# Performance work log

Measured on AMD Instinct MI355X. Metric: run time of the kernel, lower is better.

## Reference

```python
import math
import jax, jax.numpy as jnp
import numpy as np

D = 1024
B, L = 4, 4096


def _linear(x, W, b):
    # torch nn.Linear convention: y = x @ W.T + b, W: (out, in)
    return jnp.einsum('bld,ed->ble', x, W) + b


def _ma_k_activation(x, k=0.02):
    x = x / math.sqrt(x.shape[-1])
    return jax.nn.sigmoid(x * k)


def _ma_q_activation(x):
    x = -x / math.sqrt(x.shape[-1])
    return -jnp.where(x >= 0, x, 0.02 * x)  # -leaky_relu(x, 0.02)


def setup_inputs() -> dict:
    key = jax.random.key(0)
    ks = jax.random.split(key, 9)
    s = 1.0 / math.sqrt(D)
    return {
        'x': jax.random.normal(ks[0], (B, L, D), dtype=jnp.float32),
        'Wq1': jax.random.uniform(ks[1], (D, D), jnp.float32, -s, s),
        'bq1': jax.random.uniform(ks[2], (D,), jnp.float32, -s, s),
        'Wk1': jax.random.uniform(ks[3], (D, D), jnp.float32, -s, s),
        'bk1': jax.random.uniform(ks[4], (D,), jnp.float32, -s, s),
        'Wk2': jax.random.uniform(ks[5], (D, D), jnp.float32, -s, s),
        'bk2': jax.random.uniform(ks[6], (D,), jnp.float32, -s, s),
        'Wproj': jax.random.uniform(ks[7], (D, D), jnp.float32, -s, s),
        'bproj': jax.random.uniform(ks[8], (D,), jnp.float32, -s, s),
    }


def reference(x, Wq1, bq1, Wk1, bk1, Wk2, bk2, Wproj, bproj):
    V = x
    # AR branch: exponential keys, normalized running average, sigmoid query gate
    K = jnp.exp(_linear(x, Wk1, bk1))                      # (B,L,D)
    K_cum = jnp.cumsum(K, axis=1) + 1e-6
    S = jnp.cumsum(K * V, axis=1) / K_cum
    Q = jax.nn.sigmoid(_linear(x, Wq1, bq1))
    O_ar = S * Q
    # MA branch: residual errors gated by shifted (q,k) activations
    zero = jnp.zeros_like(x[:, :1, :])
    E = jnp.concatenate([zero, V[:, 1:, :] - O_ar[:, :-1, :]], axis=1)
    qk2_in = jnp.concatenate([zero, x[:, :-1, :]], axis=1)
    K2 = _ma_k_activation(_linear(qk2_in, Wk2, bk2))
    S2 = jnp.cumsum(K2 * E, axis=1)
    Q2 = _ma_q_activation(Q)
    Q2 = jnp.concatenate([zero, Q2[:, :-1, :]], axis=1)
    O_ma = S2 * Q2
    return _linear(O_ar + O_ma, Wproj, bproj)
```

## Files before the change

### kernel.cpp

```cpp
#include <hip/hip_runtime.h>

#define D_DIM 1024
#define L_DIM 4096
#define B_DIM 4
#define M_DIM (B_DIM * L_DIM)
#define N1    3072
#define KDIM  1024
#define NKT   16
#define KAPPA 6.25e-4f

using f32x4  = __attribute__((ext_vector_type(4))) float;
using bf16x8 = __attribute__((ext_vector_type(8))) short;

__device__ __forceinline__ unsigned short f2bf(float f) {
    unsigned u = __float_as_uint(f);
    u += 0x7fffu + ((u >> 16) & 1u);
    return (unsigned short)(u >> 16);
}
__device__ __forceinline__ float bf2f(unsigned short h) {
    return __uint_as_float(((unsigned)h) << 16);
}
__device__ __forceinline__ float bflo(unsigned u) { return __uint_as_float(u << 16); }
__device__ __forceinline__ float bfhi(unsigned u) { return __uint_as_float(u & 0xffff0000u); }
__device__ __forceinline__ unsigned pack2(float a, float b) {
    return (unsigned)f2bf(a) | ((unsigned)f2bf(b) << 16);
}
__device__ __forceinline__ float sigmoidf_(float x) {
    return 1.0f / (1.0f + __expf(-x));
}

__global__ void cvt_bf16_kernel(const float* __restrict__ in, unsigned short* __restrict__ out, int n) {
    int i = (blockIdx.x * blockDim.x + threadIdx.x) * 4;
    if (i < n) {
        float4 v = *reinterpret_cast<const float4*>(in + i);
        uint2 p;
        p.x = pack2(v.x, v.y);
        p.y = pack2(v.z, v.w);
        *reinterpret_cast<uint2*>(out + i) = p;
    }
}

__global__ void cvt4_bf16_kernel(const float* __restrict__ w0, const float* __restrict__ w1,
                                 const float* __restrict__ w2, const float* __restrict__ w3,
                                 unsigned short* __restrict__ out) {
    int seg = blockIdx.x >> 10;
    int lb  = blockIdx.x & 1023;
    int i   = (lb * 256 + threadIdx.x) * 4;
    const float* src = (seg == 0) ? w0 : (seg == 1) ? w1 : (seg == 2) ? w2 : w3;
    float4 v = *reinterpret_cast<const float4*>(src + i);
    uint2 p;
    p.x = pack2(v.x, v.y);
    p.y = pack2(v.z, v.w);
    *reinterpret_cast<uint2*>(out + seg * 1048576 + i) = p;
}

__device__ __forceinline__ void gld_lds16(const void* g, void* s) {
    __builtin_amdgcn_global_load_lds((const __attribute__((address_space(1))) void*)g,
                                     (__attribute__((address_space(3))) void*)s, 16, 0, 0);
}

#define BAR()  do { asm volatile("" ::: "memory"); __builtin_amdgcn_s_barrier(); asm volatile("" ::: "memory"); } while (0)
#define MFMA16(a_, b_, c_) __builtin_amdgcn_mfma_f32_16x16x32_bf16(a_, b_, c_, 0, 0, 0)

__global__ __launch_bounds__(512, 2) void gemm256(
        const unsigned short* __restrict__ A, const unsigned short* __restrict__ Bm,
        unsigned short* __restrict__ Cb, float* __restrict__ Cf,
        const float* __restrict__ bb0, const float* __restrict__ bb1, const float* __restrict__ bb2,
        int nwgDiv8, int mode) {
    extern __shared__ __align__(16) short lds[];
    const int tid  = threadIdx.x;
    const int wid  = tid >> 6, lane = tid & 63;
    const int wr   = wid >> 2, wc = wid & 3;
    const int lr   = lane & 15, kg = lane >> 4;

    int lin = blockIdx.y * 64 + blockIdx.x;
    int swz = (lin & 7) * nwgDiv8 + (lin >> 3);
    int bm = swz & 63;
    int bn = swz >> 6;
    const size_t rowA0 = (size_t)bm * 256;
    const size_t rowB0 = (size_t)bn * 256;

    const int rh = tid >> 2;
    const int sl = (tid & 3) ^ ((rh >> 1) & 3);
    const int wbase = (tid >> 6) * 512;
    const size_t aoffG = (size_t)rh * KDIM + sl * 8;

#define STAGE(Mp_, row0_, kt_, kh_, c_, mat_, cur_) \
    gld_lds16((Mp_) + ((row0_) + (size_t)(c_) * 128) * KDIM + (size_t)(kt_) * 64 + (kh_) * 32 + aoffG, \
              (void*)(lds + (cur_) * 32768 + (mat_) * 16384 + (kh_) * 8192 + (c_) * 4096 + wbase))

    const int slotR = kg ^ ((lr >> 1) & 3);
    const int aRd = (wr * 128 + lr) * 32 + slotR * 8;
    const int bRd = (wc * 64  + lr) * 32 + slotR * 8;

    f32x4 acc[8][4];
#pragma unroll
    for (int i = 0; i < 8; ++i)
#pragma unroll
        for (int j = 0; j < 4; ++j) acc[i][j] = (f32x4){0.f, 0.f, 0.f, 0.f};

    STAGE(A,  rowA0, 0, 0, 0, 0, 0); STAGE(A,  rowA0, 0, 0, 1, 0, 0);
    STAGE(Bm, rowB0, 0, 0, 0, 1, 0); STAGE(Bm, rowB0, 0, 0, 1, 1, 0);
    STAGE(A,  rowA0, 0, 1, 0, 0, 0); STAGE(A,  rowA0, 0, 1, 1, 0, 0);
    STAGE(Bm, rowB0, 0, 1, 0, 1, 0); STAGE(Bm, rowB0, 0, 1, 1, 1, 0);
    STAGE(A,  rowA0, 1, 0, 0, 0, 1); STAGE(A,  rowA0, 1, 0, 1, 0, 1);
    STAGE(Bm, rowB0, 1, 0, 0, 1, 1); STAGE(Bm, rowB0, 1, 0, 1, 1, 1);
    asm volatile("s_waitcnt vmcnt(4)" ::: "memory");
    BAR();

    for (int kt = 0; kt < NKT; ++kt) {
        const int cur = kt & 1;
        const int nc  = cur ^ 1;
        const short* A0 = lds + cur * 32768;
        const short* A1 = A0 + 8192;
        const short* B0 = A0 + 16384;
        const short* B1 = A0 + 24576;
        bf16x8 a[8], b0, b1, b2, b3;

        #pragma unroll
        for (int fm = 0; fm < 8; ++fm) a[fm] = *reinterpret_cast<const bf16x8*>(A0 + aRd + fm * 512);
        b0 = *reinterpret_cast<const bf16x8*>(B0 + bRd);
        b1 = *reinterpret_cast<const bf16x8*>(B0 + bRd + 512);
        if (kt + 1 < NKT) {
            STAGE(A, rowA0, kt + 1, 1, 0, 0, nc); STAGE(A, rowA0, kt + 1, 1, 1, 0, nc);
        }
        BAR();
        __builtin_amdgcn_s_setprio(1);
        #pragma unroll
        for (int fm = 0; fm < 8; ++fm) {
            acc[fm][0] = MFMA16(b0, a[fm], acc[fm][0]);
            acc[fm][1] = MFMA16(b1, a[fm], acc[fm][1]);
        }
        __builtin_amdgcn_s_setprio(0);
        BAR();

        b2 = *reinterpret_cast<const bf16x8*>(B0 + bRd + 1024);
        b3 = *reinterpret_cast<const bf16x8*>(B0 + bRd + 1536);
        if (kt + 1 < NKT) {
            STAGE(Bm, rowB0, kt + 1, 1, 0, 1, nc); STAGE(Bm, rowB0, kt + 1, 1, 1, 1, nc);
        }
        BAR();
        __builtin_amdgcn_s_setprio(1);
        #pragma unroll
        for (int fm = 0; fm < 8; ++fm) {
            acc[fm][2] = MFMA16(b2, a[fm], acc[fm][2]);
            acc[fm][3] = MFMA16(b3, a[fm], acc[fm][3]);
        }
        __builtin_amdgcn_s_setprio(0);
        BAR();

        #pragma unroll
        for (int fm = 0; fm < 8; ++fm) a[fm] = *reinterpret_cast<const bf16x8*>(A1 + aRd + fm * 512);
        b0 = *reinterpret_cast<const bf16x8*>(B1 + bRd);
        b1 = *reinterpret_cast<const bf16x8*>(B1 + bRd + 512);
        if (kt + 2 < NKT) {
            STAGE(A, rowA0, kt + 2, 0, 0, 0, cur); STAGE(A, rowA0, kt + 2, 0, 1, 0, cur);
        }
        BAR();
        __builtin_amdgcn_s_setprio(1);
        #pragma unroll
        for (int fm = 0; fm < 8; ++fm) {
            acc[fm][0] = MFMA16(b0, a[fm], acc[fm][0]);
            acc[fm][1] = MFMA16(b1, a[fm], acc[fm][1]);
        }
        __builtin_amdgcn_s_setprio(0);
        BAR();

        b2 = *reinterpret_cast<const bf16x8*>(B1 + bRd + 1024);
        b3 = *reinterpret_cast<const bf16x8*>(B1 + bRd + 1536);
        if (kt + 2 < NKT) {
            STAGE(Bm, rowB0, kt + 2, 0, 0, 1, cur); STAGE(Bm, rowB0, kt + 2, 0, 1, 1, cur);
        }
        BAR();
        __builtin_amdgcn_s_setprio(1);
        #pragma unroll
        for (int fm = 0; fm < 8; ++fm) {
            acc[fm][2] = MFMA16(b2, a[fm], acc[fm][2]);
            acc[fm][3] = MFMA16(b3, a[fm], acc[fm][3]);
        }
        __builtin_amdgcn_s_setprio(0);
        if (kt < NKT - 2) { asm volatile("s_waitcnt vmcnt(4)" ::: "memory"); }
        else              { asm volatile("s_waitcnt vmcnt(0)" ::: "memory"); }
        BAR();
    }

    const int rowBase = bm * 256 + wr * 128;
    const int colBase = bn * 256 + wc * 64;
    if (mode == 0) {
        const int seg = (colBase >> 10);
        const float* bs = (seg == 0) ? bb0 : ((seg == 1) ? bb1 : bb2);
#pragma unroll
        for (int fm = 0; fm < 8; ++fm) {
            int row = rowBase + fm * 16 + lr;
            unsigned short* cp = Cb + (size_t)row * 3072;
#pragma unroll
            for (int fn = 0; fn < 4; ++fn) {
                int col0 = colBase + fn * 16 + kg * 4;
                float4 b4 = *reinterpret_cast<const float4*>(bs + (col0 & 1023));
                float v0 = acc[fm][fn][0] + b4.x;
                float v1 = acc[fm][fn][1] + b4.y;
                float v2 = acc[fm][fn][2] + b4.z;
                float v3 = acc[fm][fn][3] + b4.w;
                float r0, r1, r2, r3;
                if (seg == 0)      { r0 = __expf(v0); r1 = __expf(v1); r2 = __expf(v2); r3 = __expf(v3); }
                else if (seg == 1) { r0 = sigmoidf_(v0); r1 = sigmoidf_(v1); r2 = sigmoidf_(v2); r3 = sigmoidf_(v3); }
                else               { r0 = sigmoidf_(v0 * KAPPA); r1 = sigmoidf_(v1 * KAPPA);
                                     r2 = sigmoidf_(v2 * KAPPA); r3 = sigmoidf_(v3 * KAPPA); }
                uint2 p;
                p.x = pack2(r0, r1);
                p.y = pack2(r2, r3);
                *reinterpret_cast<uint2*>(cp + col0) = p;
            }
        }
    } else {
#pragma unroll
        for (int fm = 0; fm < 8; ++fm) {
            int row = rowBase + fm * 16 + lr;
            float* cp = Cf + (size_t)row * 1024;
#pragma unroll
            for (int fn = 0; fn < 4; ++fn) {
                int col0 = colBase + fn * 16 + kg * 4;
                float4 b4 = *reinterpret_cast<const float4*>(bb0 + col0);
                float4 v;
                v.x = acc[fm][fn][0] + b4.x;
                v.y = acc[fm][fn][1] + b4.y;
                v.z = acc[fm][fn][2] + b4.z;
                v.w = acc[fm][fn][3] + b4.w;
                *reinterpret_cast<float4*>(cp + col0) = v;
            }
        }
    }
#undef STAGE
}


__global__ __launch_bounds__(256) void pass1v(
        const unsigned short* __restrict__ KQ, const unsigned short* __restrict__ xbf,
        float2* __restrict__ pK, float2* __restrict__ pKV) {
    const int thr = threadIdx.x;
    const int dq = blockIdx.x & 1;
    const int bc = blockIdx.x >> 1;
    const int b = bc >> 6, c = bc & 63;
    const int d0 = dq * 512 + thr * 2;
    const size_t row0 = (size_t)b * L_DIM + (size_t)c * 64;
    const unsigned short* kp = KQ  + row0 * 3072 + d0;
    const unsigned short* vp = xbf + row0 * 1024 + d0;
    float sK0 = 0.f, sK1 = 0.f, sKV0 = 0.f, sKV1 = 0.f;
#pragma unroll 8
    for (int t = 0; t < 64; ++t) {
        unsigned ku = *reinterpret_cast<const unsigned*>(kp + (size_t)t * 3072);
        unsigned vu = *reinterpret_cast<const unsigned*>(vp + (size_t)t * 1024);
        sK0 += bflo(ku); sK1 += bfhi(ku);
        sKV0 += bflo(ku) * bflo(vu); sKV1 += bfhi(ku) * bfhi(vu);
    }
    const size_t slot = (size_t)bc * 512 + dq * 256 + thr;
    pK[slot]  = make_float2(sK0, sK1);
    pKV[slot] = make_float2(sKV0, sKV1);
}

__global__ __launch_bounds__(256) void pass3v(
        const unsigned short* __restrict__ KQ, const unsigned short* __restrict__ xbf,
        const float2* __restrict__ pK, const float2* __restrict__ pKV,
        unsigned short* __restrict__ z, float2* __restrict__ pM) {
    const int thr = threadIdx.x;
    const int dq = blockIdx.x & 1;
    const int bc = blockIdx.x >> 1;
    const int b = bc >> 6, c = bc & 63;
    const int d0 = dq * 512 + thr * 2;
    const size_t row0 = (size_t)b * L_DIM + (size_t)c * 64;
    const unsigned short* kqp = KQ  + row0 * 3072 + d0;
    const unsigned short* vp  = xbf + row0 * 1024 + d0;
    unsigned short* zp = z + row0 * 1024 + d0;

    float cK0 = 0.f, cK1 = 0.f, cKV0 = 0.f, cKV1 = 0.f;
    const size_t base = (size_t)(b << 6) * 512 + dq * 256 + thr;
#pragma unroll 4
    for (int cp = 0; cp < c; ++cp) {
        float2 a = pK [base + (size_t)cp * 512];
        float2 q2 = pKV[base + (size_t)cp * 512];
        cK0 += a.x; cK1 += a.y; cKV0 += q2.x; cKV1 += q2.y;
    }

    float oar_prev0 = 0.f, oar_prev1 = 0.f, k2_prev0 = 0.f, k2_prev1 = 0.f;
    float q_prev0 = 0.f, q_prev1 = 0.f;
    if (c != 0) {
        unsigned qm  = *reinterpret_cast<const unsigned*>(kqp - 3072 + 1024);
        unsigned k2m = *reinterpret_cast<const unsigned*>(kqp - 3072 + 2048);
        oar_prev0 = bflo(qm) * (cKV0 / (cK0 + 1e-6f));
        oar_prev1 = bfhi(qm) * (cKV1 / (cK1 + 1e-6f));
        k2_prev0 = bflo(k2m); k2_prev1 = bfhi(k2m);
        q_prev0 = bflo(qm);   q_prev1 = bfhi(qm);
    }
    float sM0 = 0.f, sM1 = 0.f;
#pragma unroll 4
    for (int t = 0; t < 64; ++t) {
        unsigned ku  = *reinterpret_cast<const unsigned*>(kqp + (size_t)t * 3072);
        unsigned qu  = *reinterpret_cast<const unsigned*>(kqp + (size_t)t * 3072 + 1024);
        unsigned k2u = *reinterpret_cast<const unsigned*>(kqp + (size_t)t * 3072 + 2048);
        unsigned vu  = *reinterpret_cast<const unsigned*>(vp  + (size_t)t * 1024);
        float v0 = bflo(vu), v1 = bfhi(vu);
        cK0 += bflo(ku); cKV0 += bflo(ku) * v0;
        cK1 += bfhi(ku); cKV1 += bfhi(ku) * v1;
        float oar0 = bflo(qu) * (cKV0 / (cK0 + 1e-6f));
        float oar1 = bfhi(qu) * (cKV1 / (cK1 + 1e-6f));
        float m0 = k2_prev0 * (v0 - oar_prev0);
        float m1 = k2_prev1 * (v1 - oar_prev1);
        sM0 += m0; sM1 += m1;
        float z0 = oar0 + sM0 * KAPPA * q_prev0;
        float z1 = oar1 + sM1 * KAPPA * q_prev1;
        *reinterpret_cast<unsigned*>(zp + (size_t)t * 1024) = pack2(z0, z1);
        oar_prev0 = oar0; oar_prev1 = oar1;
        k2_prev0 = bflo(k2u); k2_prev1 = bfhi(k2u);
        q_prev0 = bflo(qu);   q_prev1 = bfhi(qu);
    }
    pM[(size_t)bc * 512 + dq * 256 + thr] = make_float2(sM0, sM1);
}

__global__ __launch_bounds__(256) void pass5v(
        const unsigned short* __restrict__ KQ, unsigned short* __restrict__ zy,
        const float2* __restrict__ pM) {
    const int thr = threadIdx.x;
    const int dq = blockIdx.x & 1;
    const int bc = blockIdx.x >> 1;
    const int b = bc >> 6, c = bc & 63;
    if (c == 0) return;
    const int d0 = dq * 512 + thr * 2;
    const size_t row0 = (size_t)b * L_DIM + (size_t)c * 64;

    float offM0 = 0.f, offM1 = 0.f;
    const size_t base = (size_t)(b << 6) * 512 + dq * 256 + thr;
#pragma unroll 4
    for (int cp = 0; cp < c; ++cp) {
        float2 a = pM[base + (size_t)cp * 512];
        offM0 += a.x; offM1 += a.y;
    }
    const float s0 = offM0 * KAPPA, s1 = offM1 * KAPPA;
    const unsigned short* qp = KQ + (row0 - 1) * 3072 + 1024 + d0;
    unsigned short* zp = zy + row0 * 1024 + d0;
#pragma unroll 8
    for (int t = 0; t < 64; ++t) {
        unsigned qu = *reinterpret_cast<const unsigned*>(qp + (size_t)t * 3072);
        unsigned zu = *reinterpret_cast<const unsigned*>(zp + (size_t)t * 1024);
        float y0 = bflo(zu) + s0 * bflo(qu);
        float y1 = bfhi(zu) + s1 * bfhi(qu);
        *reinterpret_cast<unsigned*>(zp + (size_t)t * 1024) = pack2(y0, y1);
    }
}

extern "C" void kernel_launch(void* const* d_in, const int* in_sizes, int n_in,
                              void* d_out, int out_size, void* d_ws, size_t ws_size,
                              hipStream_t stream) {
    (void)in_sizes; (void)n_in; (void)out_size; (void)ws_size;
    const float* x   = (const float*)d_in[0];
    const float* Wq1 = (const float*)d_in[1];
    const float* bq1 = (const float*)d_in[2];
    const float* Wk1 = (const float*)d_in[3];
    const float* bk1 = (const float*)d_in[4];
    const float* Wk2 = (const float*)d_in[5];
    const float* bk2 = (const float*)d_in[6];
    const float* Wpj = (const float*)d_in[7];
    const float* bpj = (const float*)d_in[8];
    float* out = (float*)d_out;

    char* ws = (char*)d_ws;
    unsigned short* xbf   = (unsigned short*)(ws);
    unsigned short* Wcat  = (unsigned short*)(ws + 33554432);
    unsigned short* Wpjbf = (unsigned short*)(ws + 39845888);
    unsigned short* KQ    = (unsigned short*)(ws + 41943040);
    unsigned short* zy    = (unsigned short*)(ws + 142606336);
    float2* pK  = (float2*)(ws + 176160768);
    float2* pKV = (float2*)(ws + 177209344);
    float2* pM  = (float2*)(ws + 178257920);

    (void)hipFuncSetAttribute((const void*)gemm256,
                              hipFuncAttributeMaxDynamicSharedMemorySize, 131072);

    const int nx = M_DIM * D_DIM;
    cvt_bf16_kernel<<<nx / 4 / 256, 256, 0, stream>>>(x, xbf, nx);
    cvt4_bf16_kernel<<<4096, 256, 0, stream>>>(Wk1, Wq1, Wk2, Wpj, Wcat);

    gemm256<<<dim3(64, 12), 512, 131072, stream>>>(xbf, Wcat, KQ, nullptr,
                                                   bk1, bq1, bk2, 96, 0);

    pass1v<<<512, 256, 0, stream>>>(KQ, xbf, pK, pKV);
    pass3v<<<512, 256, 0, stream>>>(KQ, xbf, pK, pKV, zy, pM);
    pass5v<<<512, 256, 0, stream>>>(KQ, zy, pM);

    gemm256<<<dim3(64, 4), 512, 131072, stream>>>(zy, Wpjbf, nullptr, out,
                                                  bpj, nullptr, nullptr, 32, 1);
}
```

Before: 263.4 us.

## Fuse chunk-level K and K*V partial sums into GEMM epilogue, drop pass1v

The exp(K) segment of the first GEMM epilogue now also reads the matching bf16 V values, reduces K and K*V over 64-row chunks with wave shuffles, and writes the per-chunk partial sums directly. This removes the separate pass1v kernel, which re-read K and V from global memory. The cost is extra V loads, shuffles and register pressure in the GEMM epilogue, plus a layout that depends on how 64-row chunks map onto the tile and wave rows.

```diff
diff --git a/kernel.cpp b/kernel.cpp
--- a/kernel.cpp
+++ b/kernel.cpp
@@ -64,8 +64,10 @@
 
 __global__ __launch_bounds__(512, 2) void gemm256(
         const unsigned short* __restrict__ A, const unsigned short* __restrict__ Bm,
+        const unsigned short* __restrict__ Xv,
         unsigned short* __restrict__ Cb, float* __restrict__ Cf,
         const float* __restrict__ bb0, const float* __restrict__ bb1, const float* __restrict__ bb2,
+        float* __restrict__ pKf, float* __restrict__ pKVf,
         int nwgDiv8, int mode) {
     extern __shared__ __align__(16) short lds[];
     const int tid  = threadIdx.x;
@@ -188,28 +190,73 @@
     const int colBase = bn * 256 + wc * 64;
     if (mode == 0) {
         const int seg = (colBase >> 10);
-        const float* bs = (seg == 0) ? bb0 : ((seg == 1) ? bb1 : bb2);
-#pragma unroll
-        for (int fm = 0; fm < 8; ++fm) {
-            int row = rowBase + fm * 16 + lr;
-            unsigned short* cp = Cb + (size_t)row * 3072;
+        if (seg == 0) {
+            const int bq = bm >> 4;
+            const size_t bcA = (size_t)bq * 64 + ((bm & 15) << 2) + (wr << 1);
 #pragma unroll
             for (int fn = 0; fn < 4; ++fn) {
-                int col0 = colBase + fn * 16 + kg * 4;
-                float4 b4 = *reinterpret_cast<const float4*>(bs + (col0 & 1023));
-                float v0 = acc[fm][fn][0] + b4.x;
-                float v1 = acc[fm][fn][1] + b4.y;
-                float v2 = acc[fm][fn][2] + b4.z;
-                float v3 = acc[fm][fn][3] + b4.w;
-                float r0, r1, r2, r3;
-                if (seg == 0)      { r0 = __expf(v0); r1 = __expf(v1); r2 = __expf(v2); r3 = __expf(v3); }
-                else if (seg == 1) { r0 = sigmoidf_(v0); r1 = sigmoidf_(v1); r2 = sigmoidf_(v2); r3 = sigmoidf_(v3); }
-                else               { r0 = sigmoidf_(v0 * KAPPA); r1 = sigmoidf_(v1 * KAPPA);
-                                     r2 = sigmoidf_(v2 * KAPPA); r3 = sigmoidf_(v3 * KAPPA); }
-                uint2 p;
-                p.x = pack2(r0, r1);
-                p.y = pack2(r2, r3);
-                *reinterpret_cast<uint2*>(cp + col0) = p;
+                const int col0 = colBase + fn * 16 + kg * 4;
+                float4 b4 = *reinterpret_cast<const float4*>(bb0 + col0);
+                float sk0 = 0.f, sk1 = 0.f, sk2 = 0.f, sk3 = 0.f;
+                float sv0 = 0.f, sv1 = 0.f, sv2 = 0.f, sv3 = 0.f;
+#pragma unroll
+                for (int fm = 0; fm < 8; ++fm) {
+                    const int row = rowBase + fm * 16 + lr;
+                    float r0 = __expf(acc[fm][fn][0] + b4.x);
+                    float r1 = __expf(acc[fm][fn][1] + b4.y);
+                    float r2 = __expf(acc[fm][fn][2] + b4.z);
+                    float r3 = __expf(acc[fm][fn][3] + b4.w);
+                    uint2 p;
+                    p.x = pack2(r0, r1);
+                    p.y = pack2(r2, r3);
+                    *reinterpret_cast<uint2*>(Cb + (size_t)row * 3072 + col0) = p;
+                    uint2 vv = *reinterpret_cast<const uint2*>(Xv + (size_t)row * 1024 + col0);
+                    sk0 += r0; sk1 += r1; sk2 += r2; sk3 += r3;
+                    sv0 += r0 * bflo(vv.x); sv1 += r1 * bfhi(vv.x);
+                    sv2 += r2 * bflo(vv.y); sv3 += r3 * bfhi(vv.y);
+                    if (fm == 3 || fm == 7) {
+#pragma unroll
+                        for (int msk = 1; msk < 16; msk <<= 1) {
+                            sk0 += __shfl_xor(sk0, msk); sk1 += __shfl_xor(sk1, msk);
+                            sk2 += __shfl_xor(sk2, msk); sk3 += __shfl_xor(sk3, msk);
+                            sv0 += __shfl_xor(sv0, msk); sv1 += __shfl_xor(sv1, msk);
+                            sv2 += __shfl_xor(sv2, msk); sv3 += __shfl_xor(sv3, msk);
+                        }
+                        if (lr == 0) {
+                            const size_t bc = (fm == 3) ? bcA : bcA + 1;
+                            float4 fk; fk.x = sk0; fk.y = sk1; fk.z = sk2; fk.w = sk3;
+                            float4 fv; fv.x = sv0; fv.y = sv1; fv.z = sv2; fv.w = sv3;
+                            *reinterpret_cast<float4*>(pKf  + bc * 1024 + col0) = fk;
+                            *reinterpret_cast<float4*>(pKVf + bc * 1024 + col0) = fv;
+                        }
+                        sk0 = sk1 = sk2 = sk3 = 0.f;
+                        sv0 = sv1 = sv2 = sv3 = 0.f;
+                    }
+                }
+            }
+        } else {
+            const float* bs = (seg == 1) ? bb1 : bb2;
+#pragma unroll
+            for (int fm = 0; fm < 8; ++fm) {
+                int row = rowBase + fm * 16 + lr;
+                unsigned short* cp = Cb + (size_t)row * 3072;
+#pragma unroll
+                for (int fn = 0; fn < 4; ++fn) {
+                    int col0 = colBase + fn * 16 + kg * 4;
+                    float4 b4 = *reinterpret_cast<const float4*>(bs + (col0 & 1023));
+                    float v0 = acc[fm][fn][0] + b4.x;
+                    float v1 = acc[fm][fn][1] + b4.y;
+                    float v2 = acc[fm][fn][2] + b4.z;
+                    float v3 = acc[fm][fn][3] + b4.w;
+                    float r0, r1, r2, r3;
+                    if (seg == 1) { r0 = sigmoidf_(v0); r1 = sigmoidf_(v1); r2 = sigmoidf_(v2); r3 = sigmoidf_(v3); }
+                    else          { r0 = sigmoidf_(v0 * KAPPA); r1 = sigmoidf_(v1 * KAPPA);
+                                    r2 = sigmoidf_(v2 * KAPPA); r3 = sigmoidf_(v3 * KAPPA); }
+                    uint2 p;
+                    p.x = pack2(r0, r1);
+                    p.y = pack2(r2, r3);
+                    *reinterpret_cast<uint2*>(cp + col0) = p;
+                }
             }
         }
     } else {
@@ -233,30 +280,6 @@
 #undef STAGE
 }
 
-
-__global__ __launch_bounds__(256) void pass1v(
-        const unsigned short* __restrict__ KQ, const unsigned short* __restrict__ xbf,
-        float2* __restrict__ pK, float2* __restrict__ pKV) {
-    const int thr = threadIdx.x;
-    const int dq = blockIdx.x & 1;
-    const int bc = blockIdx.x >> 1;
-    const int b = bc >> 6, c = bc & 63;
-    const int d0 = dq * 512 + thr * 2;
-    const size_t row0 = (size_t)b * L_DIM + (size_t)c * 64;
-    const unsigned short* kp = KQ  + row0 * 3072 + d0;
-    const unsigned short* vp = xbf + row0 * 1024 + d0;
-    float sK0 = 0.f, sK1 = 0.f, sKV0 = 0.f, sKV1 = 0.f;
-#pragma unroll 8
-    for (int t = 0; t < 64; ++t) {
-        unsigned ku = *reinterpret_cast<const unsigned*>(kp + (size_t)t * 3072);
-        unsigned vu = *reinterpret_cast<const unsigned*>(vp + (size_t)t * 1024);
-        sK0 += bflo(ku); sK1 += bfhi(ku);
-        sKV0 += bflo(ku) * bflo(vu); sKV1 += bfhi(ku) * bfhi(vu);
-    }
-    const size_t slot = (size_t)bc * 512 + dq * 256 + thr;
-    pK[slot]  = make_float2(sK0, sK1);
-    pKV[slot] = make_float2(sKV0, sKV1);
-}
 
 __global__ __launch_bounds__(256) void pass3v(
         const unsigned short* __restrict__ KQ, const unsigned short* __restrict__ xbf,
@@ -368,8 +391,8 @@
     unsigned short* Wpjbf = (unsigned short*)(ws + 39845888);
     unsigned short* KQ    = (unsigned short*)(ws + 41943040);
     unsigned short* zy    = (unsigned short*)(ws + 142606336);
-    float2* pK  = (float2*)(ws + 176160768);
-    float2* pKV = (float2*)(ws + 177209344);
+    float* pKf  = (float*)(ws + 176160768);
+    float* pKVf = (float*)(ws + 177209344);
     float2* pM  = (float2*)(ws + 178257920);
 
     (void)hipFuncSetAttribute((const void*)gemm256,
@@ -379,13 +402,12 @@
     cvt_bf16_kernel<<<nx / 4 / 256, 256, 0, stream>>>(x, xbf, nx);
     cvt4_bf16_kernel<<<4096, 256, 0, stream>>>(Wk1, Wq1, Wk2, Wpj, Wcat);
 
-    gemm256<<<dim3(64, 12), 512, 131072, stream>>>(xbf, Wcat, KQ, nullptr,
-                                                   bk1, bq1, bk2, 96, 0);
-
-    pass1v<<<512, 256, 0, stream>>>(KQ, xbf, pK, pKV);
-    pass3v<<<512, 256, 0, stream>>>(KQ, xbf, pK, pKV, zy, pM);
+    gemm256<<<dim3(64, 12), 512, 131072, stream>>>(xbf, Wcat, xbf, KQ, nullptr,
+                                                   bk1, bq1, bk2, pKf, pKVf, 96, 0);
+
+    pass3v<<<512, 256, 0, stream>>>(KQ, xbf, (const float2*)pKf, (const float2*)pKVf, zy, pM);
     pass5v<<<512, 256, 0, stream>>>(KQ, zy, pM);
 
-    gemm256<<<dim3(64, 4), 512, 131072, stream>>>(zy, Wpjbf, nullptr, out,
-                                                  bpj, nullptr, nullptr, 32, 1);
-}
+    gemm256<<<dim3(64, 4), 512, 131072, stream>>>(zy, Wpjbf, nullptr, nullptr, out,
+                                                  bpj, nullptr, nullptr, nullptr, nullptr, 32, 1);
+}
```

Result: slower. 280.1 us (+6.3%).
